# Kernel optimization log

Hardware: AMD Instinct MI355X
Metric: run time of the kernel (lower is better)

## Reference

```python
import jax, jax.numpy as jnp
import numpy as np

DT = 0.1


def _gru_step(x, h, wih, whh, bih, bhh):
    # x: [B,R,I], h: [B,R,H], wih: [R,3H,I], whh: [R,3H,H]
    H = h.shape[-1]
    gi = jnp.einsum('bri,rji->brj', x, wih) + bih
    gh = jnp.einsum('brh,rjh->brj', h, whh) + bhh
    i_r, i_z, i_n = gi[..., :H], gi[..., H:2 * H], gi[..., 2 * H:]
    h_r, h_z, h_n = gh[..., :H], gh[..., H:2 * H], gh[..., 2 * H:]
    reset = jax.nn.sigmoid(i_r + h_r)
    update = jax.nn.sigmoid(i_z + h_z)
    new = jnp.tanh(i_n + reset * h_n)
    return (1 - update) * new + update * h


def _flow(state, cond, gsw, gsb, gcw, lw, lb, ow, ob):
    # gated-relaxation FINDR-style flow, R parallel MLPs (einsum 'bri,roi->bro')
    gate = jax.nn.sigmoid(jnp.einsum('bri,roi->bro', state, gsw) + gsb
                          + jnp.einsum('bri,roi->bro', cond, gcw))
    h = jnp.concatenate([state, cond], axis=-1)          # [B,R,2L]
    h = jax.nn.silu(jnp.einsum('bri,roi->bro', h, lw) + lb)
    target = jnp.tanh(jnp.einsum('bri,roi->bro', h, ow) + ob)
    return gate * (-state + target)


def setup_inputs() -> dict:
    key = jax.random.key(0)
    B, R, L, M, Hh, Hf, T = 64, 12, 32, 16, 32, 64, 200
    pairs = [(s, t) for s in range(R) for t in range(R) if s != t]
    E = len(pairs)  # 132 directed inter-region edges
    src_idx = jnp.array([s for s, _ in pairs], dtype=jnp.int32)
    tgt_idx = jnp.array([t for _, t in pairs], dtype=jnp.int32)
    ks = jax.random.split(key, 12)

    def xav(k, shape):
        fan = shape[-1] + shape[-2]
        return jax.random.normal(k, shape, jnp.float32) * np.sqrt(2.0 / fan)

    return {
        'z0': jax.random.normal(ks[0], (B, R, L), jnp.float32),
        'h0': jax.random.normal(ks[1], (B, R, Hh), jnp.float32),
        'mean_w': xav(ks[2], (E, M, L)),
        'mean_b': jnp.zeros((E, M), jnp.float32),
        'add_w': 0.1 * jax.random.normal(ks[3], (E, L, M), jnp.float32),
        'gate_state_w': xav(ks[4], (R, L, L)),
        'gate_state_b': jnp.zeros((R, L), jnp.float32),
        'gate_cond_w': xav(ks[5], (R, L, L)),
        'layer_w': xav(ks[6], (R, Hf, 2 * L)),
        'layer_b': jnp.zeros((R, Hf), jnp.float32),
        'out_w': xav(ks[7], (R, L, Hf)),
        'out_b': jnp.zeros((R, L), jnp.float32),
        'wih': xav(ks[8], (R, 3 * Hh, L)),
        'whh': xav(ks[9], (R, 3 * Hh, Hh)),
        'bih': jnp.zeros((R, 3 * Hh), jnp.float32),
        'bhh': jnp.zeros((R, 3 * Hh), jnp.float32),
        'src_idx': src_idx,
        'tgt_idx': tgt_idx,
        'n_steps': T,
    }


def reference(z0, h0, mean_w, mean_b, add_w,
              gate_state_w, gate_state_b, gate_cond_w,
              layer_w, layer_b, out_w, out_b,
              wih, whh, bih, bhh, src_idx, tgt_idx, n_steps):
    def step(carry, _):
        z, h = carry
        src = z[:, src_idx]                                   # gather [B,E,L]
        mean = jnp.einsum('bes,ems->bem', src, mean_w) + mean_b  # edge messages
        add = jnp.einsum('bem,elm->bel', mean, add_w)         # [B,E,L]
        inc_add = jnp.zeros_like(z).at[:, tgt_idx].add(add)   # scatter-add -> [B,R,L]
        drift = _flow(z, inc_add, gate_state_w, gate_state_b, gate_cond_w,
                      layer_w, layer_b, out_w, out_b)
        h_new = _gru_step(inc_add, h, wih, whh, bih, bhh)
        z_new = z + DT * drift
        return (z_new, h_new), (z_new, mean)

    (z_f, h_f), (z_traj, msgs) = jax.lax.scan(step, (z0, h0), None, length=n_steps)
    # z_traj: [T,B,R,L] -> [B,T,R,L]; msgs: [T,B,E,M] -> [B,T,E,M]
    return z_traj.transpose(1, 0, 2, 3), h_f, msgs.transpose(1, 0, 2, 3)
```

## Files before the change

kernel.cpp:

```cpp
#include <hip/hip_runtime.h>


constexpr int R  = 12;
constexpr int L  = 32;
constexpr int M  = 16;
constexpr int HH = 32;
constexpr int HF = 64;
constexpr int E  = 132;
constexpr int G3 = 96;
constexpr float DT = 0.1f;

constexpr int G  = 4;
constexpr int BS = 512;
constexpr int ZR = 36;
constexpr int ZG = R * ZR;
constexpr int IS = 36;

typedef float f4v __attribute__((ext_vector_type(4)));

__device__ __forceinline__ float sigmoidf(float x) {
    return 1.0f / (1.0f + __expf(-x));
}
__device__ __forceinline__ float fma4(float4 a, float4 x, float acc) {
    acc = fmaf(a.x, x.x, acc);
    acc = fmaf(a.y, x.y, acc);
    acc = fmaf(a.z, x.z, acc);
    return fmaf(a.w, x.w, acc);
}

__device__ __forceinline__ void sync_lds() {
    asm volatile("s_waitcnt lgkmcnt(0)" ::: "memory");
    __builtin_amdgcn_s_barrier();
    asm volatile("" ::: "memory");
}

__global__ __launch_bounds__(BS)
__attribute__((amdgpu_waves_per_eu(2, 2)))
void nv_main(
    const float* __restrict__ z0,     const float* __restrict__ h0,
    const float* __restrict__ mean_w, const float* __restrict__ mean_b,
    const float* __restrict__ add_w,
    const float* __restrict__ gsw,    const float* __restrict__ gsb,
    const float* __restrict__ gcw,
    const float* __restrict__ lw,     const float* __restrict__ lb,
    const float* __restrict__ ow_w,   const float* __restrict__ ob,
    const float* __restrict__ wih,    const float* __restrict__ whh,
    const float* __restrict__ bih,    const float* __restrict__ bhh,
    const int* __restrict__ src_idx,  const int* __restrict__ tgt_idx,
    const int* __restrict__ n_steps_p,
    float* __restrict__ zx,
    float* __restrict__ out, int B)
{
    const int r   = blockIdx.x;
    const int grp = blockIdx.y;
    const int tid = threadIdx.x;
    const int T   = n_steps_p[0];
    const int b0  = grp * G;
    const size_t ZXN = (size_t)B * (R * L);

    float* __restrict__ out_z    = out;
    float* __restrict__ out_hf   = out + (size_t)B * T * R * L;
    float* __restrict__ out_msgs = out_hf + (size_t)B * R * HH;

    __shared__ __align__(16) float wadd_s[11 * L * M];
    __shared__ __align__(16) float wih_s[G3 * L];
    __shared__ __align__(16) float zS[G * ZG];
    __shared__ __align__(16) float hSS[G * HH];
    __shared__ __align__(16) float meanS[G * 11 * M];
    __shared__ __align__(16) float incS[G * IS];
    __shared__ __align__(16) float gateS[G * L];
    __shared__ __align__(16) float shSS[G * HF];
    __shared__ __align__(16) float giSS[G * G3];
    __shared__ __align__(16) float ghSS[G * G3];
    __shared__ int edgeE[11], edgeSrc[11];

    if (tid == 0) {
        int c = 0;
        for (int e = 0; e < E; ++e)
            if (tgt_idx[e] == r) { edgeE[c] = e; edgeSrc[c] = src_idx[e]; ++c; }
    }
    __syncthreads();

    float4 wbuf[32];
    float biasA = 0.f, biasB = 0.f, biasC = 0.f;

    if (tid < 352) {
        const int rowl = tid % 176;
        const int el = rowl >> 4, m = rowl & 15;
        const int row = edgeE[el] * M + m;
        const float4* p = (const float4*)(mean_w + (size_t)row * L);
#pragma unroll
        for (int k = 0; k < 8; ++k) wbuf[k] = p[k];
        biasA = mean_b[row];
    }
    if (tid >= 384 && tid < 480) {
        const int j = tid - 384, row = r * G3 + j;
        const float4* p = (const float4*)(whh + (size_t)row * HH);
#pragma unroll
        for (int k = 0; k < 8; ++k) wbuf[k] = p[k];
        biasA = bhh[row];
    }
    if (tid < 256) {
        const int j = tid & 63, row = r * HF + j;
        const float4* p = (const float4*)(lw + (size_t)row * 2 * L);
#pragma unroll
        for (int k = 0; k < 16; ++k) wbuf[8 + k] = p[k];
        biasB = lb[row];
    }
    if (tid >= 256 && tid < 384) {
        const int j = (tid - 256) & 31, row = r * L + j;
        const float4* pa = (const float4*)(gsw + (size_t)row * L);
        const float4* pb = (const float4*)(gcw + (size_t)row * L);
#pragma unroll
        for (int k = 0; k < 8; ++k) { wbuf[8 + k] = pa[k]; wbuf[16 + k] = pb[k]; }
        biasB = gsb[row];
    }
    if (tid >= 384) {
        const int j = (tid - 384) & 31, row = r * L + j;
        const float4* p = (const float4*)(ow_w + (size_t)row * HF);
#pragma unroll
        for (int k = 0; k < 16; ++k) wbuf[8 + k] = p[k];
        biasB = ob[row];
    }
    if (tid >= 128) {
        const int j = (tid - 128) % 96;
        biasC = bih[r * G3 + j];
    }

    for (int i = tid; i < 11 * L * M; i += BS) {
        const int e = i >> 9, rem = i & 511, l = rem >> 4, m = rem & 15;
        wadd_s[((e * 4 + (m >> 2)) * 32 + l) * 4 + (m & 3)] =
            add_w[((size_t)edgeE[e] * L + l) * M + m];
    }
    for (int i = tid; i < G3 * L; i += BS) {
        const int j = i >> 5, cw = i & 31, c = cw >> 2, w = cw & 3;
        wih_s[j * 32 + ((c ^ (j & 7)) << 2) + w] = wih[(size_t)r * G3 * L + i];
    }

    for (int i = tid; i < G * R * L; i += BS) {
        const int g = i / (R * L), rl = i - g * (R * L);
        const int room = rl >> 5, l = rl & 31;
        zS[g * ZG + room * ZR + l] = z0[(size_t)(b0 + g) * R * L + rl];
    }
    for (int i = tid; i < G * HH; i += BS) {
        const int g = i >> 5, hh = i & 31;
        hSS[i] = h0[(size_t)(b0 + g) * R * HH + r * HH + hh];
    }
    __syncthreads();

    const float NANF = __uint_as_float(0xFFFFFFFFu);

    for (int t = 0; t < T; ++t) {
        if (tid < 352) {
            const int rowl = tid % 176;
            const int sr = edgeSrc[rowl >> 4];
            const int gb = (tid < 176) ? 0 : 2;
#pragma unroll
            for (int gg = 0; gg < 2; ++gg) {
                const int g = gb + gg;
                const float4* zp = (const float4*)(zS + g * ZG + sr * ZR);
                float a = biasA;
#pragma unroll
                for (int c = 0; c < 8; ++c) a = fma4(wbuf[c], zp[c], a);
                meanS[g * 176 + rowl] = a;
            }
        } else if (tid >= 480 && t >= 1) {
            float* __restrict__ zq = zx + (size_t)((t - 1) % 3) * ZXN;
            const int i = tid - 480;
            const int g = i >> 3, l4 = i & 7;
            float* pp = zq + (size_t)(b0 + g) * (R * L) + r * L + l4 * 4;
#pragma unroll
            for (int w = 0; w < 4; ++w)
                __hip_atomic_store(pp + w, NANF, __ATOMIC_RELAXED,
                                   __HIP_MEMORY_SCOPE_AGENT);
        }
        sync_lds();

        if (tid < 128) {
            const int g = tid >> 5, l = tid & 31;
            const float4* mp = (const float4*)(meanS + g * 176);
            const float4* wp = (const float4*)wadd_s;
            float a = 0.f;
#pragma unroll
            for (int e = 0; e < 11; ++e)
#pragma unroll
                for (int c = 0; c < 4; ++c)
                    a = fma4(wp[(e * 4 + c) * 32 + l], mp[e * 4 + c], a);
            incS[g * IS + l] = a;
        } else if (tid < 304) {
            const int k = tid - 128;
            const int g = k / 44, i = k - g * 44;
            const int el = i >> 2, m4 = i & 3;
            const f4v v = *(const f4v*)(meanS + g * 176 + i * 4);
            __builtin_nontemporal_store(
                v, (f4v*)&out_msgs[((size_t)(b0 + g) * T + t) * (E * M)
                                   + edgeE[el] * 16 + m4 * 4]);
        } else if (tid >= 384 && tid < 480) {
            const int j = tid - 384;
#pragma unroll
            for (int g = 0; g < G; ++g) {
                const float4* hp = (const float4*)(hSS + g * HH);
                float a = biasA;
#pragma unroll
                for (int c = 0; c < 8; ++c) a = fma4(wbuf[c], hp[c], a);
                ghSS[g * G3 + j] = a;
            }
        } else if (tid >= 480) {
            asm volatile("s_waitcnt vmcnt(0)" ::: "memory");
        }
        sync_lds();

        if (tid < 256) {
            const int j = tid & 63, g = tid >> 6;
            const float4* zp = (const float4*)(zS + g * ZG + r * ZR);
            const float4* ip = (const float4*)(incS + g * IS);
            float a = biasB;
#pragma unroll
            for (int c = 0; c < 8; ++c) {
                a = fma4(wbuf[8 + c], zp[c], a);
                a = fma4(wbuf[16 + c], ip[c], a);
            }
            shSS[g * HF + j] = a * sigmoidf(a);
        } else if (tid < 384) {
            const int k = tid - 256;
            const int j = k & 31, g = k >> 5;
            const float4* zp = (const float4*)(zS + g * ZG + r * ZR);
            const float4* ip = (const float4*)(incS + g * IS);
            float a = biasB;
#pragma unroll
            for (int c = 0; c < 8; ++c) {
                a = fma4(wbuf[8 + c], zp[c], a);
                a = fma4(wbuf[16 + c], ip[c], a);
            }
            gateS[g * L + j] = sigmoidf(a);
        }
        if (tid >= 128) {
            const int k = tid - 128;
            const int j = k % 96, g = k / 96;
            const float* wb = wih_s + j * 32;
            const int jx = j & 7;
            const float4* ip = (const float4*)(incS + g * IS);
            float a = biasC;
#pragma unroll
            for (int c = 0; c < 8; ++c)
                a = fma4(*(const float4*)(wb + ((c ^ jx) << 2)), ip[c], a);
            giSS[g * G3 + j] = a;
        }
        sync_lds();

        float* __restrict__ zxp = zx + (size_t)((t + 1) % 3) * ZXN;
        if (tid >= 384) {
            const int k = tid - 384;
            const int j = k & 31, g = k >> 5;
            const float4* sp = (const float4*)(shSS + g * HF);
            float a = biasB;
#pragma unroll
            for (int c = 0; c < 16; ++c) a = fma4(wbuf[8 + c], sp[c], a);
            const float target = tanhf(a);
            const float zv = zS[g * ZG + r * ZR + j];
            const float znew = zv + DT * gateS[g * L + j] * (target - zv);
            zS[g * ZG + r * ZR + j] = znew;
            if (t + 1 < T)
                __hip_atomic_store(&zxp[(size_t)(b0 + g) * (R * L) + r * L + j],
                                   znew, __ATOMIC_RELAXED,
                                   __HIP_MEMORY_SCOPE_AGENT);
            __builtin_nontemporal_store(
                znew, &out_z[((size_t)(b0 + g) * T + t) * (R * L) + r * L + j]);
        } else {
            if (tid >= 256) {
                const int i = tid - 256;
                const int g = i >> 5, hh = i & 31;
                const float ir  = giSS[g * G3 + hh];
                const float iz  = giSS[g * G3 + HH + hh];
                const float inn = giSS[g * G3 + 2 * HH + hh];
                const float hr  = ghSS[g * G3 + hh];
                const float hz  = ghSS[g * G3 + HH + hh];
                const float hnv = ghSS[g * G3 + 2 * HH + hh];
                const float reset = sigmoidf(ir + hr);
                const float upd   = sigmoidf(iz + hz);
                const float nw    = tanhf(inn + reset * hnv);
                hSS[g * HH + hh] = (1.0f - upd) * nw + upd * hSS[g * HH + hh];
            }
            if (tid < 352 && t + 1 < T) {
                const int team = tid >> 5, rem = tid & 31;
                const int s    = team + (team >= r ? 1 : 0);
                const int g    = rem >> 3, l4 = rem & 7;
                const float* sp =
                    zxp + (size_t)(b0 + g) * (R * L) + s * L + l4 * 4;
                float4 v;
                for (;;) {
                    v.x = __hip_atomic_load(sp + 0, __ATOMIC_RELAXED, __HIP_MEMORY_SCOPE_AGENT);
                    v.y = __hip_atomic_load(sp + 1, __ATOMIC_RELAXED, __HIP_MEMORY_SCOPE_AGENT);
                    v.z = __hip_atomic_load(sp + 2, __ATOMIC_RELAXED, __HIP_MEMORY_SCOPE_AGENT);
                    v.w = __hip_atomic_load(sp + 3, __ATOMIC_RELAXED, __HIP_MEMORY_SCOPE_AGENT);
                    if (v.x == v.x && v.y == v.y && v.z == v.z && v.w == v.w)
                        break;
                    __builtin_amdgcn_s_sleep(1);
                }
                *(float4*)(zS + g * ZG + s * ZR + l4 * 4) = v;
            }
        }
        sync_lds();
    }

    for (int i = tid; i < G * HH; i += BS) {
        const int g = i >> 5, hh = i & 31;
        __builtin_nontemporal_store(
            hSS[i], &out_hf[(size_t)(b0 + g) * R * HH + r * HH + hh]);
    }
}

extern "C" void kernel_launch(void* const* d_in, const int* in_sizes, int n_in,
                              void* d_out, int out_size, void* d_ws, size_t ws_size,
                              hipStream_t stream) {
    const float* z0     = (const float*)d_in[0];
    const float* h0     = (const float*)d_in[1];
    const float* mean_w = (const float*)d_in[2];
    const float* mean_b = (const float*)d_in[3];
    const float* add_w  = (const float*)d_in[4];
    const float* gsw    = (const float*)d_in[5];
    const float* gsb    = (const float*)d_in[6];
    const float* gcw    = (const float*)d_in[7];
    const float* lw     = (const float*)d_in[8];
    const float* lb     = (const float*)d_in[9];
    const float* ow_w   = (const float*)d_in[10];
    const float* ob     = (const float*)d_in[11];
    const float* wih    = (const float*)d_in[12];
    const float* whh    = (const float*)d_in[13];
    const float* bih    = (const float*)d_in[14];
    const float* bhh    = (const float*)d_in[15];
    const int* src_idx  = (const int*)d_in[16];
    const int* tgt_idx  = (const int*)d_in[17];
    const int* n_steps  = (const int*)d_in[18];

    const int B  = in_sizes[0] / (R * L);
    const int NG = B / G;

    float* zx = (float*)d_ws;

    (void)hipMemsetAsync(zx, 0xFF, (size_t)3 * B * R * L * sizeof(float), stream);

    nv_main<<<dim3(R, NG), dim3(BS), 72000, stream>>>(
        z0, h0, mean_w, mean_b, add_w, gsw, gsb, gcw, lw, lb, ow_w, ob,
        wih, whh, bih, bhh, src_idx, tgt_idx, n_steps,
        zx, (float*)d_out, B);
}
```

Before: 903.1 us.

## Rebalance per-step work across warps and pad shared arrays to avoid bank conflicts

Moves the GRU hidden-to-hidden matvec into the first phase alongside the mean computation, and moves the message output stores into the last phase alongside the GRU update. It also pads the LDS rows for h, gate, silu hidden and gate pre-activations with extra columns, and adds a short sleep for warps waiting before the cross-block poll. The goal is to balance work per barrier phase, cut LDS bank conflicts and reduce the critical path per time step. The trade-off is a slightly longer first and last phase and changed polling timing.

```diff
diff --git a/kernel.cpp b/kernel.cpp
--- a/kernel.cpp
+++ b/kernel.cpp
@@ -15,6 +15,10 @@
 constexpr int ZR = 36;
 constexpr int ZG = R * ZR;
 constexpr int IS = 36;
+constexpr int HS = 36;
+constexpr int SH = 68;
+constexpr int GS = 36;
+constexpr int GG = 100;
 
 typedef float f4v __attribute__((ext_vector_type(4)));
 
@@ -65,13 +69,13 @@
     __shared__ __align__(16) float wadd_s[11 * L * M];
     __shared__ __align__(16) float wih_s[G3 * L];
     __shared__ __align__(16) float zS[G * ZG];
-    __shared__ __align__(16) float hSS[G * HH];
+    __shared__ __align__(16) float hSS[G * HS];
     __shared__ __align__(16) float meanS[G * 11 * M];
     __shared__ __align__(16) float incS[G * IS];
-    __shared__ __align__(16) float gateS[G * L];
-    __shared__ __align__(16) float shSS[G * HF];
-    __shared__ __align__(16) float giSS[G * G3];
-    __shared__ __align__(16) float ghSS[G * G3];
+    __shared__ __align__(16) float gateS[G * GS];
+    __shared__ __align__(16) float shSS[G * SH];
+    __shared__ __align__(16) float giSS[G * GG];
+    __shared__ __align__(16) float ghSS[G * GG];
     __shared__ int edgeE[11], edgeSrc[11];
 
     if (tid == 0) {
@@ -144,7 +148,7 @@
     }
     for (int i = tid; i < G * HH; i += BS) {
         const int g = i >> 5, hh = i & 31;
-        hSS[i] = h0[(size_t)(b0 + g) * R * HH + r * HH + hh];
+        hSS[g * HS + hh] = h0[(size_t)(b0 + g) * R * HH + r * HH + hh];
     }
     __syncthreads();
 
@@ -164,6 +168,16 @@
                 for (int c = 0; c < 8; ++c) a = fma4(wbuf[c], zp[c], a);
                 meanS[g * 176 + rowl] = a;
             }
+        } else if (tid >= 384 && tid < 480) {
+            const int j = tid - 384;
+#pragma unroll
+            for (int g = 0; g < G; ++g) {
+                const float4* hp = (const float4*)(hSS + g * HS);
+                float a = biasA;
+#pragma unroll
+                for (int c = 0; c < 8; ++c) a = fma4(wbuf[c], hp[c], a);
+                ghSS[g * GG + j] = a;
+            }
         } else if (tid >= 480 && t >= 1) {
             float* __restrict__ zq = zx + (size_t)((t - 1) % 3) * ZXN;
             const int i = tid - 480;
@@ -187,24 +201,6 @@
                 for (int c = 0; c < 4; ++c)
                     a = fma4(wp[(e * 4 + c) * 32 + l], mp[e * 4 + c], a);
             incS[g * IS + l] = a;
-        } else if (tid < 304) {
-            const int k = tid - 128;
-            const int g = k / 44, i = k - g * 44;
-            const int el = i >> 2, m4 = i & 3;
-            const f4v v = *(const f4v*)(meanS + g * 176 + i * 4);
-            __builtin_nontemporal_store(
-                v, (f4v*)&out_msgs[((size_t)(b0 + g) * T + t) * (E * M)
-                                   + edgeE[el] * 16 + m4 * 4]);
-        } else if (tid >= 384 && tid < 480) {
-            const int j = tid - 384;
-#pragma unroll
-            for (int g = 0; g < G; ++g) {
-                const float4* hp = (const float4*)(hSS + g * HH);
-                float a = biasA;
-#pragma unroll
-                for (int c = 0; c < 8; ++c) a = fma4(wbuf[c], hp[c], a);
-                ghSS[g * G3 + j] = a;
-            }
         } else if (tid >= 480) {
             asm volatile("s_waitcnt vmcnt(0)" ::: "memory");
         }
@@ -220,7 +216,7 @@
                 a = fma4(wbuf[8 + c], zp[c], a);
                 a = fma4(wbuf[16 + c], ip[c], a);
             }
-            shSS[g * HF + j] = a * sigmoidf(a);
+            shSS[g * SH + j] = a * sigmoidf(a);
         } else if (tid < 384) {
             const int k = tid - 256;
             const int j = k & 31, g = k >> 5;
@@ -232,7 +228,7 @@
                 a = fma4(wbuf[8 + c], zp[c], a);
                 a = fma4(wbuf[16 + c], ip[c], a);
             }
-            gateS[g * L + j] = sigmoidf(a);
+            gateS[g * GS + j] = sigmoidf(a);
         }
         if (tid >= 128) {
             const int k = tid - 128;
@@ -244,7 +240,7 @@
 #pragma unroll
             for (int c = 0; c < 8; ++c)
                 a = fma4(*(const float4*)(wb + ((c ^ jx) << 2)), ip[c], a);
-            giSS[g * G3 + j] = a;
+            giSS[g * GG + j] = a;
         }
         sync_lds();
 
@@ -252,13 +248,13 @@
         if (tid >= 384) {
             const int k = tid - 384;
             const int j = k & 31, g = k >> 5;
-            const float4* sp = (const float4*)(shSS + g * HF);
+            const float4* sp = (const float4*)(shSS + g * SH);
             float a = biasB;
 #pragma unroll
             for (int c = 0; c < 16; ++c) a = fma4(wbuf[8 + c], sp[c], a);
             const float target = tanhf(a);
             const float zv = zS[g * ZG + r * ZR + j];
-            const float znew = zv + DT * gateS[g * L + j] * (target - zv);
+            const float znew = zv + DT * gateS[g * GS + j] * (target - zv);
             zS[g * ZG + r * ZR + j] = znew;
             if (t + 1 < T)
                 __hip_atomic_store(&zxp[(size_t)(b0 + g) * (R * L) + r * L + j],
@@ -267,19 +263,28 @@
             __builtin_nontemporal_store(
                 znew, &out_z[((size_t)(b0 + g) * T + t) * (R * L) + r * L + j]);
         } else {
-            if (tid >= 256) {
-                const int i = tid - 256;
+            if (tid < 176) {
+                const int g = tid / 44, i = tid - g * 44;
+                const int el = i >> 2, m4 = i & 3;
+                const f4v v = *(const f4v*)(meanS + g * 176 + i * 4);
+                __builtin_nontemporal_store(
+                    v, (f4v*)&out_msgs[((size_t)(b0 + g) * T + t) * (E * M)
+                                       + edgeE[el] * 16 + m4 * 4]);
+            } else if (tid < 304) {
+                const int i = tid - 176;
                 const int g = i >> 5, hh = i & 31;
-                const float ir  = giSS[g * G3 + hh];
-                const float iz  = giSS[g * G3 + HH + hh];
-                const float inn = giSS[g * G3 + 2 * HH + hh];
-                const float hr  = ghSS[g * G3 + hh];
-                const float hz  = ghSS[g * G3 + HH + hh];
-                const float hnv = ghSS[g * G3 + 2 * HH + hh];
+                const float ir  = giSS[g * GG + hh];
+                const float iz  = giSS[g * GG + HH + hh];
+                const float inn = giSS[g * GG + 2 * HH + hh];
+                const float hr  = ghSS[g * GG + hh];
+                const float hz  = ghSS[g * GG + HH + hh];
+                const float hnv = ghSS[g * GG + 2 * HH + hh];
                 const float reset = sigmoidf(ir + hr);
                 const float upd   = sigmoidf(iz + hz);
                 const float nw    = tanhf(inn + reset * hnv);
-                hSS[g * HH + hh] = (1.0f - upd) * nw + upd * hSS[g * HH + hh];
+                hSS[g * HS + hh] = (1.0f - upd) * nw + upd * hSS[g * HS + hh];
+            } else if (tid < 352) {
+                if (t + 1 < T) __builtin_amdgcn_s_sleep(4);
             }
             if (tid < 352 && t + 1 < T) {
                 const int team = tid >> 5, rem = tid & 31;
@@ -306,7 +311,7 @@
     for (int i = tid; i < G * HH; i += BS) {
         const int g = i >> 5, hh = i & 31;
         __builtin_nontemporal_store(
-            hSS[i], &out_hf[(size_t)(b0 + g) * R * HH + r * HH + hh]);
+            hSS[g * HS + hh], &out_hf[(size_t)(b0 + g) * R * HH + r * HH + hh]);
     }
 }
 
```

Measured after the change: 957.0 us. 1.06x slower.
